# Performance work log

Hardware: AMD Instinct MI355X
Metric: run time of the kernel (lower is better)

Reference implementation:

```python
import jax, jax.numpy as jnp
import numpy as np

CHEB_K = 3

def setup_inputs() -> dict:
    key = jax.random.key(0)
    k1, k2, k3, k4 = jax.random.split(key, 4)
    B, N, C_IN, C_OUT, D = 64, 2048, 64, 64, 16
    return {
        "x": jax.random.normal(k1, (B, N, C_IN), dtype=jnp.float32),
        "node_embeddings": jax.random.normal(k2, (N, D), dtype=jnp.float32),
        "weights_pool": jax.random.normal(k3, (D, CHEB_K, C_IN, C_OUT), dtype=jnp.float32) * 0.1,
        "bias_pool": jax.random.normal(k4, (D, C_OUT), dtype=jnp.float32) * 0.1,
    }

def reference(x, node_embeddings, weights_pool, bias_pool):
    # x: [B, N, C_in]; node_embeddings: [N, D]
    N = node_embeddings.shape[0]
    # adaptive adjacency: row-softmax of relu(E E^T)
    supports = jax.nn.softmax(jax.nn.relu(node_embeddings @ node_embeddings.T), axis=1)
    # Chebyshev polynomial recursion: T0 = I, T1 = A, Tk = 2 A T_{k-1} - T_{k-2}
    support_set = [jnp.eye(N, dtype=x.dtype), supports]
    for _ in range(2, CHEB_K):
        support_set.append(2.0 * supports @ support_set[-1] - support_set[-2])
    supports_stack = jnp.stack(support_set, axis=0)  # [K, N, N]
    # per-node generated weights/bias from embedding pools
    weights = jnp.einsum('nd,dkio->nkio', node_embeddings, weights_pool)  # [N, K, C_in, C_out]
    bias = node_embeddings @ bias_pool  # [N, C_out]
    # graph convolution: aggregate then per-node GEMM
    x_g = jnp.einsum('knm,bmc->bknc', supports_stack, x)  # [B, K, N, C_in]
    out = jnp.einsum('bkni,nkio->bno', x_g, weights) + bias  # [B, N, C_out]
    return out
```

## Files before the change

### kernel.cpp

```cpp
#include <hip/hip_runtime.h>
#include <hip/hip_bf16.h>
#include <stdint.h>

using bf16   = __bf16;
using bf16x8 = __attribute__((ext_vector_type(8))) __bf16;
using f32x2  = __attribute__((ext_vector_type(2))) float;
using f32x4  = __attribute__((ext_vector_type(4))) float;

#define NN  2048
#define DD  16
#define BB  64
#define CC  64
#define BCC 4096
#define GNODE 2

__device__ inline float4 f4max(float4 a, float4 b) {
  return make_float4(fmaxf(a.x,b.x), fmaxf(a.y,b.y), fmaxf(a.z,b.z), fmaxf(a.w,b.w));
}
__device__ inline float4 f4add(float4 a, float4 b) {
  return make_float4(a.x+b.x, a.y+b.y, a.z+b.z, a.w+b.w);
}

__global__ __launch_bounds__(256) void k_softmax(const float* __restrict__ E,
                                                 bf16* __restrict__ A) {
  const int n0 = blockIdx.x * 4;
  const int t = threadIdx.x;
  float en[4][DD];
#pragma unroll
  for (int g = 0; g < 4; ++g)
#pragma unroll
    for (int d = 0; d < DD; ++d) en[g][d] = E[(size_t)(n0 + g) * DD + d];

  float4 r[8];
  float4 mx = make_float4(0.f, 0.f, 0.f, 0.f);
#pragma unroll
  for (int j = 0; j < 8; ++j) {
    const int m = t + 256 * j;
    const float4* ep = (const float4*)(E + (size_t)m * DD);
    float4 p0 = ep[0], p1 = ep[1], p2 = ep[2], p3 = ep[3];
    float s[4];
#pragma unroll
    for (int g = 0; g < 4; ++g) {
      s[g] = p0.x*en[g][0] + p0.y*en[g][1] + p0.z*en[g][2] + p0.w*en[g][3]
           + p1.x*en[g][4] + p1.y*en[g][5] + p1.z*en[g][6] + p1.w*en[g][7]
           + p2.x*en[g][8] + p2.y*en[g][9] + p2.z*en[g][10] + p2.w*en[g][11]
           + p3.x*en[g][12]+ p3.y*en[g][13]+ p3.z*en[g][14]+ p3.w*en[g][15];
      s[g] = fmaxf(s[g], 0.0f);
    }
    r[j] = make_float4(s[0], s[1], s[2], s[3]);
    mx = f4max(mx, r[j]);
  }
  __shared__ float4 red[256];
  red[t] = mx;
  __syncthreads();
  for (int off = 128; off > 0; off >>= 1) {
    if (t < off) red[t] = f4max(red[t], red[t + off]);
    __syncthreads();
  }
  mx = red[0];
  __syncthreads();
  float4 ex[8];
  float4 sum = make_float4(0.f, 0.f, 0.f, 0.f);
#pragma unroll
  for (int j = 0; j < 8; ++j) {
    ex[j] = make_float4(__expf(r[j].x - mx.x), __expf(r[j].y - mx.y),
                        __expf(r[j].z - mx.z), __expf(r[j].w - mx.w));
    sum = f4add(sum, ex[j]);
  }
  red[t] = sum;
  __syncthreads();
  for (int off = 128; off > 0; off >>= 1) {
    if (t < off) red[t] = f4add(red[t], red[t + off]);
    __syncthreads();
  }
  const float4 tot = red[0];
  const float inv[4] = {1.f/tot.x, 1.f/tot.y, 1.f/tot.z, 1.f/tot.w};
#pragma unroll
  for (int j = 0; j < 8; ++j) {
    const int m = t + 256 * j;
    A[(size_t)(n0 + 0) * NN + m] = (bf16)(ex[j].x * inv[0]);
    A[(size_t)(n0 + 1) * NN + m] = (bf16)(ex[j].y * inv[1]);
    A[(size_t)(n0 + 2) * NN + m] = (bf16)(ex[j].z * inv[2]);
    A[(size_t)(n0 + 3) * NN + m] = (bf16)(ex[j].w * inv[3]);
  }
}

__global__ __launch_bounds__(256) void k_transpose(const bf16* __restrict__ in,
                                                   bf16* __restrict__ out,
                                                   int R, int C) {
  __shared__ bf16 tile[64 * 68];
  const int bx = blockIdx.x, by = blockIdx.y;
  const int t = threadIdx.x;
  const int r0 = by * 64, c0 = bx * 64;
#pragma unroll
  for (int j = 0; j < 16; ++j) {
    const int q = t + 256 * j;
    const int r = q >> 6, c = q & 63;
    tile[r * 68 + c] = in[(size_t)(r0 + r) * C + c0 + c];
  }
  __syncthreads();
#pragma unroll
  for (int j = 0; j < 16; ++j) {
    const int q = t + 256 * j;
    const int rr = q >> 6, cc = q & 63;
    out[(size_t)(c0 + rr) * R + r0 + cc] = tile[cc * 68 + rr];
  }
}

__global__ __launch_bounds__(256) void k_build_xrt(const float* __restrict__ x,
                                                   bf16* __restrict__ XrT) {
  __shared__ bf16 tile[64 * 68];
  const int b = blockIdx.x;
  const int m0 = blockIdx.y * 64;
  const int t = threadIdx.x;
#pragma unroll
  for (int j = 0; j < 16; ++j) {
    const int q = t + 256 * j;
    const int m = q >> 6, i = q & 63;
    tile[m * 68 + i] = (bf16)x[((size_t)b * NN + m0 + m) * CC + i];
  }
  __syncthreads();
#pragma unroll
  for (int j = 0; j < 16; ++j) {
    const int q = t + 256 * j;
    const int i = q >> 6, m = q & 63;
    XrT[((size_t)b * CC + i) * NN + m0 + m] = tile[m * 68 + i];
  }
}

__global__ __launch_bounds__(256) void k_prep_wpt(const float* __restrict__ Wp,
                                                  bf16* __restrict__ WpT) {
  const int e = blockIdx.x * 256 + threadIdx.x;
  const int r = e >> 6, o = e & 63;
  const size_t src = (size_t)(r >> 6) * 4096 + (size_t)(r & 63) * 64 + o;
#pragma unroll
  for (int d = 0; d < DD; ++d)
    WpT[(size_t)e * DD + d] = (bf16)Wp[(size_t)d * 12288 + src];
}

template <int EPI>
__global__ __launch_bounds__(256) void k_gemm_bt(const bf16* __restrict__ L,
                                                 const bf16* __restrict__ R,
                                                 bf16* __restrict__ C,
                                                 int M, int Nc, int K,
                                                 const float* __restrict__ Xext,
                                                 bf16* __restrict__ CT) {
  __shared__ uint4 lds[4096];
  const int t = threadIdx.x;
  const int lane = t & 63, w = t >> 6;
  const int wm = w & 1, wn = w >> 1;
  const int h = lane >> 4;

  const int nwg = gridDim.x * gridDim.y;
  const int bid = blockIdx.y * gridDim.x + blockIdx.x;
  int bx, by;
  if (gridDim.x == 32 && gridDim.y == 16) {
    const int xcd = bid & 7, j = bid >> 3;
    bx = (xcd & 3) * 8 + (j & 7);
    by = (xcd >> 2) * 8 + (j >> 3);
  } else {
    const int cpx = nwg >> 3;
    const int swz = (bid & 7) * cpx + (bid >> 3);
    bx = swz % gridDim.x;
    by = swz / gridDim.x;
  }

  const int m0 = by * 128, n0 = bx * 128;

  f32x4 acc[4][4];
  const f32x4 zz = {0.f, 0.f, 0.f, 0.f};
#pragma unroll
  for (int mt = 0; mt < 4; ++mt)
#pragma unroll
    for (int nt = 0; nt < 4; ++nt) acc[mt][nt] = zz;

  auto stage = [&](int buf, int kt) {
    uint4* base = lds + buf * 2048;
#pragma unroll
    for (int c = 0; c < 4; ++c) {
      const int q = t + 256 * c;
      const int row = q >> 3, col4 = q & 7;
      const int scol = col4 ^ (row & 7);
      const bf16* srcL = L + (size_t)(m0 + row) * K + kt + (scol << 3);
      const bf16* srcR = R + (size_t)(n0 + row) * K + kt + (scol << 3);
      __builtin_amdgcn_global_load_lds(srcL, &base[q & ~63], 16, 0, 0);
      __builtin_amdgcn_global_load_lds(srcR, &base[1024 + (q & ~63)], 16, 0, 0);
    }
  };

  auto compute = [&](int buf) {
    const bf16x8* Lsv = (const bf16x8*)(lds + buf * 2048);
    const bf16x8* Rsv = (const bf16x8*)(lds + buf * 2048 + 1024);
#pragma unroll
    for (int kk = 0; kk < 2; ++kk) {
      bf16x8 af[4], bfr[4];
#pragma unroll
      for (int mt = 0; mt < 4; ++mt) {
        const int row = wm * 64 + mt * 16 + (lane & 15);
        af[mt] = Lsv[(row << 3) | ((kk * 4 + h) ^ (row & 7))];
      }
#pragma unroll
      for (int nt = 0; nt < 4; ++nt) {
        const int row = wn * 64 + nt * 16 + (lane & 15);
        bfr[nt] = Rsv[(row << 3) | ((kk * 4 + h) ^ (row & 7))];
      }
#pragma unroll
      for (int mt = 0; mt < 4; ++mt)
#pragma unroll
        for (int nt = 0; nt < 4; ++nt)
          acc[mt][nt] = __builtin_amdgcn_mfma_f32_16x16x32_bf16(
              af[mt], bfr[nt], acc[mt][nt], 0, 0, 0);
    }
  };

  const int NT = K >> 6;
  stage(0, 0);
  int cur = 0;
  for (int ts = 0; ts < NT - 1; ++ts) {
    stage(cur ^ 1, (ts + 1) << 6);
    asm volatile("s_waitcnt vmcnt(8)" ::: "memory");
    __builtin_amdgcn_s_barrier();
    __builtin_amdgcn_sched_barrier(0);
    compute(cur);
    __builtin_amdgcn_s_barrier();
    __builtin_amdgcn_sched_barrier(0);
    cur ^= 1;
  }
  asm volatile("s_waitcnt vmcnt(0)" ::: "memory");
  __builtin_amdgcn_s_barrier();
  __builtin_amdgcn_sched_barrier(0);
  compute(cur);

#pragma unroll
  for (int mt = 0; mt < 4; ++mt)
#pragma unroll
    for (int nt = 0; nt < 4; ++nt)
#pragma unroll
      for (int r = 0; r < 4; ++r) {
        const int rg = m0 + wm * 64 + mt * 16 + 4 * h + r;
        const int cg = n0 + wn * 64 + nt * 16 + (lane & 15);
        float v = acc[mt][nt][r];
        if (EPI == 2) {
          const int b = cg >> 6, i = cg & 63;
          v = 2.0f * v - Xext[(((size_t)b * NN + rg) * CC) + i];
        }
        C[(size_t)rg * Nc + cg] = (bf16)v;
      }

  if (EPI == 1) {
    __syncthreads();
    bf16* T = (bf16*)lds;
#pragma unroll
    for (int mt = 0; mt < 4; ++mt)
#pragma unroll
      for (int nt = 0; nt < 4; ++nt)
#pragma unroll
        for (int r = 0; r < 4; ++r) {
          const int rloc = wm * 64 + mt * 16 + 4 * h + r;
          const int cloc = wn * 64 + nt * 16 + (lane & 15);
          T[cloc * 136 + rloc] = (bf16)acc[mt][nt][r];
        }
    __syncthreads();
    const int cloc = t >> 1, half = t & 1;
#pragma unroll
    for (int jj = 0; jj < 8; ++jj) {
      const bf16x8 v = *(const bf16x8*)(T + cloc * 136 + half * 64 + jj * 8);
      *(bf16x8*)(CT + (size_t)(n0 + cloc) * M + m0 + half * 64 + jj * 8) = v;
    }
  }
}

__global__ __launch_bounds__(256) void k_node(const float* __restrict__ x,
                                              const float* __restrict__ E,
                                              const bf16* __restrict__ WpT,
                                              const float* __restrict__ bp,
                                              const bf16* __restrict__ xg1,
                                              const bf16* __restrict__ xg2,
                                              float* __restrict__ out) {
  __shared__ alignas(16) bf16 sW[GNODE * 1536 * 8];
  const int t = threadIdx.x;
  const int lane = t & 63, w = t >> 6;
  const int h = lane >> 4, l16 = lane & 15;
  const int n0 = blockIdx.x * GNODE;
  const int b = w * 16 + l16;

  float4  xa[GNODE][4];
  bf16x8  xgr[GNODE][4];
#pragma unroll
  for (int g = 0; g < GNODE; ++g) {
    const int n = n0 + g;
    const float* xb = x + ((size_t)b * NN + n) * CC;
    xa[g][0] = *(const float4*)(xb + h * 8);
    xa[g][1] = *(const float4*)(xb + h * 8 + 4);
    xa[g][2] = *(const float4*)(xb + 32 + h * 8);
    xa[g][3] = *(const float4*)(xb + 32 + h * 8 + 4);
    const bf16* x1 = xg1 + (size_t)n * BCC + b * CC;
    const bf16* x2 = xg2 + (size_t)n * BCC + b * CC;
    xgr[g][0] = *(const bf16x8*)(x1 + h * 8);
    xgr[g][1] = *(const bf16x8*)(x1 + 32 + h * 8);
    xgr[g][2] = *(const bf16x8*)(x2 + h * 8);
    xgr[g][3] = *(const bf16x8*)(x2 + 32 + h * 8);
  }

  f32x2 en2[DD];
  float en[GNODE][DD];
#pragma unroll
  for (int g = 0; g < GNODE; ++g)
#pragma unroll
    for (int d = 0; d < DD; ++d) en[g][d] = E[(size_t)(n0 + g) * DD + d];
#pragma unroll
  for (int d = 0; d < DD; ++d) en2[d] = (f32x2){en[0][d], en[1][d]};

  float bias_v[GNODE][4];
#pragma unroll
  for (int g = 0; g < GNODE; ++g)
#pragma unroll
    for (int nt = 0; nt < 4; ++nt) {
      const int o = nt * 16 + l16;
      float a = 0.0f;
#pragma unroll
      for (int d = 0; d < DD; ++d) a += en[g][d] * bp[d * CC + o];
      bias_v[g][nt] = a;
    }

#pragma unroll
  for (int c = 0; c < 6; ++c) {
    const int idx = t + 256 * c;
    const int o = idx & 63;
    const int u = idx >> 6;
    const bf16* src = WpT + ((size_t)(u * 8) * 64 + o) * DD;
    bf16x8 wv[GNODE];
#pragma unroll
    for (int j = 0; j < 8; ++j) {
      const bf16x8* wr = (const bf16x8*)(src + (size_t)j * 64 * DD);
      bf16x8 w0 = wr[0], w1 = wr[1];
      f32x2 a2 = {0.f, 0.f};
#pragma unroll
      for (int d = 0; d < 8; ++d) {
        const float wf = (float)w0[d];
        a2 += (f32x2){wf, wf} * en2[d];
      }
#pragma unroll
      for (int d = 0; d < 8; ++d) {
        const float wf = (float)w1[d];
        a2 += (f32x2){wf, wf} * en2[8 + d];
      }
      wv[0][j] = (bf16)a2[0];
      wv[1][j] = (bf16)a2[1];
    }
    const int swz = o * 24 + (u & ~7) + ((u & 7) ^ (o & 7));
#pragma unroll
    for (int g = 0; g < GNODE; ++g)
      *(bf16x8*)(sW + (size_t)(g * 1536 + swz) * 8) = wv[g];
  }
  __syncthreads();

#pragma unroll
  for (int g = 0; g < GNODE; ++g) {
    f32x4 acc[4];
    const f32x4 zz = {0.f, 0.f, 0.f, 0.f};
#pragma unroll
    for (int nt = 0; nt < 4; ++nt) acc[nt] = zz;
#pragma unroll
    for (int s = 0; s < 6; ++s) {
      bf16x8 af;
      if (s < 2) {
        const float4 u4 = xa[g][s * 2], v4 = xa[g][s * 2 + 1];
        af[0] = (bf16)u4.x; af[1] = (bf16)u4.y; af[2] = (bf16)u4.z; af[3] = (bf16)u4.w;
        af[4] = (bf16)v4.x; af[5] = (bf16)v4.y; af[6] = (bf16)v4.z; af[7] = (bf16)v4.w;
      } else {
        af = xgr[g][s - 2];
      }
      const int u = s * 4 + h;
#pragma unroll
      for (int nt = 0; nt < 4; ++nt) {
        const int o = nt * 16 + l16;
        const bf16x8 bfr = *(const bf16x8*)(
            sW + (size_t)(g * 1536 + o * 24 + (u & ~7) + ((u & 7) ^ (o & 7))) * 8);
        acc[nt] = __builtin_amdgcn_mfma_f32_16x16x32_bf16(af, bfr, acc[nt], 0, 0, 0);
      }
    }
#pragma unroll
    for (int nt = 0; nt < 4; ++nt) {
      const int o = nt * 16 + l16;
#pragma unroll
      for (int r = 0; r < 4; ++r) {
        const int br = w * 16 + 4 * h + r;
        out[((size_t)br * NN + (n0 + g)) * CC + o] = acc[nt][r] + bias_v[g][nt];
      }
    }
  }
}

extern "C" void kernel_launch(void* const* d_in, const int* in_sizes, int n_in,
                              void* d_out, int out_size, void* d_ws, size_t ws_size,
                              hipStream_t stream) {
  const float* x  = (const float*)d_in[0];
  const float* E  = (const float*)d_in[1];
  const float* Wp = (const float*)d_in[2];
  const float* bp = (const float*)d_in[3];
  float* out = (float*)d_out;

  char* ws = (char*)d_ws;
  const size_t MB = (size_t)1 << 20;
  bf16* A    = (bf16*)(ws);
  bf16* XrT  = (bf16*)(ws + 8 * MB);
  bf16* xg1  = (bf16*)(ws + 24 * MB);
  bf16* xg2  = (bf16*)(ws + 40 * MB);
  bf16* WpT  = (bf16*)(ws + 56 * MB);

  k_softmax<<<NN / 4, 256, 0, stream>>>(E, A);
  k_build_xrt<<<dim3(64, 32), 256, 0, stream>>>(x, XrT);
  k_prep_wpt<<<48, 256, 0, stream>>>(Wp, WpT);

  if (ws_size >= 80 * MB) {
    bf16* Xg1T = (bf16*)(ws + 60 * MB);
    k_gemm_bt<1><<<dim3(32, 16), 256, 0, stream>>>(A, XrT, xg1, NN, BCC, NN,
                                                   nullptr, Xg1T);
    k_gemm_bt<2><<<dim3(32, 16), 256, 0, stream>>>(A, Xg1T, xg2, NN, BCC, NN,
                                                   x, nullptr);
  } else {
    bf16* Xg1T = XrT;
    k_gemm_bt<0><<<dim3(32, 16), 256, 0, stream>>>(A, XrT, xg1, NN, BCC, NN,
                                                   nullptr, nullptr);
    k_transpose<<<dim3(64, 32), 256, 0, stream>>>(xg1, Xg1T, NN, BCC);
    k_gemm_bt<2><<<dim3(32, 16), 256, 0, stream>>>(A, Xg1T, xg2, NN, BCC, NN,
                                                   x, nullptr);
  }
  k_node<<<NN / GNODE, 256, 0, stream>>>(x, E, WpT, bp, xg1, xg2, out);
}
```

Measured before the change: 136.8 us.

## Fuse prep kernels into one launch and halve k_node shared memory

Merges the softmax, x transpose/cast and weight-pool transpose kernels into a single launch that dispatches on block index, removing two kernel launches and their gaps. In k_node, the shared-memory weight buffer now holds one node instead of two. The second node's generated weights are kept in registers and written to LDS after the first node's MFMA pass, with extra barriers. A launch bound of 4 blocks per SM is added to raise occupancy, at the risk of register pressure and the added synchronisation.

```diff
diff --git a/kernel.cpp b/kernel.cpp
--- a/kernel.cpp
+++ b/kernel.cpp
@@ -12,7 +12,6 @@
 #define BB  64
 #define CC  64
 #define BCC 4096
-#define GNODE 2
 
 __device__ inline float4 f4max(float4 a, float4 b) {
   return make_float4(fmaxf(a.x,b.x), fmaxf(a.y,b.y), fmaxf(a.z,b.z), fmaxf(a.w,b.w));
@@ -21,67 +20,101 @@
   return make_float4(a.x+b.x, a.y+b.y, a.z+b.z, a.w+b.w);
 }
 
-__global__ __launch_bounds__(256) void k_softmax(const float* __restrict__ E,
-                                                 bf16* __restrict__ A) {
-  const int n0 = blockIdx.x * 4;
+__global__ __launch_bounds__(256) void k_prep_fused(const float* __restrict__ E,
+                                                    bf16* __restrict__ A,
+                                                    const float* __restrict__ x,
+                                                    bf16* __restrict__ XrT,
+                                                    const float* __restrict__ Wp,
+                                                    bf16* __restrict__ WpT) {
+  __shared__ alignas(16) char smem[64 * 68 * 2];
+  const int blk = blockIdx.x;
   const int t = threadIdx.x;
-  float en[4][DD];
-#pragma unroll
-  for (int g = 0; g < 4; ++g)
-#pragma unroll
-    for (int d = 0; d < DD; ++d) en[g][d] = E[(size_t)(n0 + g) * DD + d];
-
-  float4 r[8];
-  float4 mx = make_float4(0.f, 0.f, 0.f, 0.f);
-#pragma unroll
-  for (int j = 0; j < 8; ++j) {
-    const int m = t + 256 * j;
-    const float4* ep = (const float4*)(E + (size_t)m * DD);
-    float4 p0 = ep[0], p1 = ep[1], p2 = ep[2], p3 = ep[3];
-    float s[4];
-#pragma unroll
-    for (int g = 0; g < 4; ++g) {
-      s[g] = p0.x*en[g][0] + p0.y*en[g][1] + p0.z*en[g][2] + p0.w*en[g][3]
-           + p1.x*en[g][4] + p1.y*en[g][5] + p1.z*en[g][6] + p1.w*en[g][7]
-           + p2.x*en[g][8] + p2.y*en[g][9] + p2.z*en[g][10] + p2.w*en[g][11]
-           + p3.x*en[g][12]+ p3.y*en[g][13]+ p3.z*en[g][14]+ p3.w*en[g][15];
-      s[g] = fmaxf(s[g], 0.0f);
-    }
-    r[j] = make_float4(s[0], s[1], s[2], s[3]);
-    mx = f4max(mx, r[j]);
-  }
-  __shared__ float4 red[256];
-  red[t] = mx;
-  __syncthreads();
-  for (int off = 128; off > 0; off >>= 1) {
-    if (t < off) red[t] = f4max(red[t], red[t + off]);
-    __syncthreads();
-  }
-  mx = red[0];
-  __syncthreads();
-  float4 ex[8];
-  float4 sum = make_float4(0.f, 0.f, 0.f, 0.f);
-#pragma unroll
-  for (int j = 0; j < 8; ++j) {
-    ex[j] = make_float4(__expf(r[j].x - mx.x), __expf(r[j].y - mx.y),
-                        __expf(r[j].z - mx.z), __expf(r[j].w - mx.w));
-    sum = f4add(sum, ex[j]);
-  }
-  red[t] = sum;
-  __syncthreads();
-  for (int off = 128; off > 0; off >>= 1) {
-    if (t < off) red[t] = f4add(red[t], red[t + off]);
-    __syncthreads();
-  }
-  const float4 tot = red[0];
-  const float inv[4] = {1.f/tot.x, 1.f/tot.y, 1.f/tot.z, 1.f/tot.w};
-#pragma unroll
-  for (int j = 0; j < 8; ++j) {
-    const int m = t + 256 * j;
-    A[(size_t)(n0 + 0) * NN + m] = (bf16)(ex[j].x * inv[0]);
-    A[(size_t)(n0 + 1) * NN + m] = (bf16)(ex[j].y * inv[1]);
-    A[(size_t)(n0 + 2) * NN + m] = (bf16)(ex[j].z * inv[2]);
-    A[(size_t)(n0 + 3) * NN + m] = (bf16)(ex[j].w * inv[3]);
+
+  if (blk < 512) {
+    float4* red = (float4*)smem;
+    const int n0 = blk * 4;
+    float en[4][DD];
+#pragma unroll
+    for (int g = 0; g < 4; ++g)
+#pragma unroll
+      for (int d = 0; d < DD; ++d) en[g][d] = E[(size_t)(n0 + g) * DD + d];
+
+    float4 r[8];
+    float4 mx = make_float4(0.f, 0.f, 0.f, 0.f);
+#pragma unroll
+    for (int j = 0; j < 8; ++j) {
+      const int m = t + 256 * j;
+      const float4* ep = (const float4*)(E + (size_t)m * DD);
+      float4 p0 = ep[0], p1 = ep[1], p2 = ep[2], p3 = ep[3];
+      float s[4];
+#pragma unroll
+      for (int g = 0; g < 4; ++g) {
+        s[g] = p0.x*en[g][0] + p0.y*en[g][1] + p0.z*en[g][2] + p0.w*en[g][3]
+             + p1.x*en[g][4] + p1.y*en[g][5] + p1.z*en[g][6] + p1.w*en[g][7]
+             + p2.x*en[g][8] + p2.y*en[g][9] + p2.z*en[g][10] + p2.w*en[g][11]
+             + p3.x*en[g][12]+ p3.y*en[g][13]+ p3.z*en[g][14]+ p3.w*en[g][15];
+        s[g] = fmaxf(s[g], 0.0f);
+      }
+      r[j] = make_float4(s[0], s[1], s[2], s[3]);
+      mx = f4max(mx, r[j]);
+    }
+    red[t] = mx;
+    __syncthreads();
+    for (int off = 128; off > 0; off >>= 1) {
+      if (t < off) red[t] = f4max(red[t], red[t + off]);
+      __syncthreads();
+    }
+    mx = red[0];
+    __syncthreads();
+    float4 ex[8];
+    float4 sum = make_float4(0.f, 0.f, 0.f, 0.f);
+#pragma unroll
+    for (int j = 0; j < 8; ++j) {
+      ex[j] = make_float4(__expf(r[j].x - mx.x), __expf(r[j].y - mx.y),
+                          __expf(r[j].z - mx.z), __expf(r[j].w - mx.w));
+      sum = f4add(sum, ex[j]);
+    }
+    red[t] = sum;
+    __syncthreads();
+    for (int off = 128; off > 0; off >>= 1) {
+      if (t < off) red[t] = f4add(red[t], red[t + off]);
+      __syncthreads();
+    }
+    const float4 tot = red[0];
+    const float inv[4] = {1.f/tot.x, 1.f/tot.y, 1.f/tot.z, 1.f/tot.w};
+#pragma unroll
+    for (int j = 0; j < 8; ++j) {
+      const int m = t + 256 * j;
+      A[(size_t)(n0 + 0) * NN + m] = (bf16)(ex[j].x * inv[0]);
+      A[(size_t)(n0 + 1) * NN + m] = (bf16)(ex[j].y * inv[1]);
+      A[(size_t)(n0 + 2) * NN + m] = (bf16)(ex[j].z * inv[2]);
+      A[(size_t)(n0 + 3) * NN + m] = (bf16)(ex[j].w * inv[3]);
+    }
+  } else if (blk < 2560) {
+    bf16* tile = (bf16*)smem;
+    const int q0 = blk - 512;
+    const int b = q0 >> 5;
+    const int m0 = (q0 & 31) * 64;
+#pragma unroll
+    for (int j = 0; j < 16; ++j) {
+      const int q = t + 256 * j;
+      const int m = q >> 6, i = q & 63;
+      tile[m * 68 + i] = (bf16)x[((size_t)b * NN + m0 + m) * CC + i];
+    }
+    __syncthreads();
+#pragma unroll
+    for (int j = 0; j < 16; ++j) {
+      const int q = t + 256 * j;
+      const int i = q >> 6, m = q & 63;
+      XrT[((size_t)b * CC + i) * NN + m0 + m] = tile[m * 68 + i];
+    }
+  } else {
+    const int e = (blk - 2560) * 256 + t;
+    const int r = e >> 6, o = e & 63;
+    const size_t src = (size_t)(r >> 6) * 4096 + (size_t)(r & 63) * 64 + o;
+#pragma unroll
+    for (int d = 0; d < DD; ++d)
+      WpT[(size_t)e * DD + d] = (bf16)Wp[(size_t)d * 12288 + src];
   }
 }
 
@@ -105,37 +138,6 @@
     const int rr = q >> 6, cc = q & 63;
     out[(size_t)(c0 + rr) * R + r0 + cc] = tile[cc * 68 + rr];
   }
-}
-
-__global__ __launch_bounds__(256) void k_build_xrt(const float* __restrict__ x,
-                                                   bf16* __restrict__ XrT) {
-  __shared__ bf16 tile[64 * 68];
-  const int b = blockIdx.x;
-  const int m0 = blockIdx.y * 64;
-  const int t = threadIdx.x;
-#pragma unroll
-  for (int j = 0; j < 16; ++j) {
-    const int q = t + 256 * j;
-    const int m = q >> 6, i = q & 63;
-    tile[m * 68 + i] = (bf16)x[((size_t)b * NN + m0 + m) * CC + i];
-  }
-  __syncthreads();
-#pragma unroll
-  for (int j = 0; j < 16; ++j) {
-    const int q = t + 256 * j;
-    const int i = q >> 6, m = q & 63;
-    XrT[((size_t)b * CC + i) * NN + m0 + m] = tile[m * 68 + i];
-  }
-}
-
-__global__ __launch_bounds__(256) void k_prep_wpt(const float* __restrict__ Wp,
-                                                  bf16* __restrict__ WpT) {
-  const int e = blockIdx.x * 256 + threadIdx.x;
-  const int r = e >> 6, o = e & 63;
-  const size_t src = (size_t)(r >> 6) * 4096 + (size_t)(r & 63) * 64 + o;
-#pragma unroll
-  for (int d = 0; d < DD; ++d)
-    WpT[(size_t)e * DD + d] = (bf16)Wp[(size_t)d * 12288 + src];
 }
 
 template <int EPI>
@@ -270,24 +272,24 @@
   }
 }
 
-__global__ __launch_bounds__(256) void k_node(const float* __restrict__ x,
-                                              const float* __restrict__ E,
-                                              const bf16* __restrict__ WpT,
-                                              const float* __restrict__ bp,
-                                              const bf16* __restrict__ xg1,
-                                              const bf16* __restrict__ xg2,
-                                              float* __restrict__ out) {
-  __shared__ alignas(16) bf16 sW[GNODE * 1536 * 8];
+__global__ __launch_bounds__(256, 4) void k_node(const float* __restrict__ x,
+                                                 const float* __restrict__ E,
+                                                 const bf16* __restrict__ WpT,
+                                                 const float* __restrict__ bp,
+                                                 const bf16* __restrict__ xg1,
+                                                 const bf16* __restrict__ xg2,
+                                                 float* __restrict__ out) {
+  __shared__ alignas(16) bf16 sW[1536 * 8];
   const int t = threadIdx.x;
   const int lane = t & 63, w = t >> 6;
   const int h = lane >> 4, l16 = lane & 15;
-  const int n0 = blockIdx.x * GNODE;
+  const int n0 = blockIdx.x * 2;
   const int b = w * 16 + l16;
 
-  float4  xa[GNODE][4];
-  bf16x8  xgr[GNODE][4];
-#pragma unroll
-  for (int g = 0; g < GNODE; ++g) {
+  float4  xa[2][4];
+  bf16x8  xgr[2][4];
+#pragma unroll
+  for (int g = 0; g < 2; ++g) {
     const int n = n0 + g;
     const float* xb = x + ((size_t)b * NN + n) * CC;
     xa[g][0] = *(const float4*)(xb + h * 8);
@@ -303,17 +305,17 @@
   }
 
   f32x2 en2[DD];
-  float en[GNODE][DD];
-#pragma unroll
-  for (int g = 0; g < GNODE; ++g)
+  float en[2][DD];
+#pragma unroll
+  for (int g = 0; g < 2; ++g)
 #pragma unroll
     for (int d = 0; d < DD; ++d) en[g][d] = E[(size_t)(n0 + g) * DD + d];
 #pragma unroll
   for (int d = 0; d < DD; ++d) en2[d] = (f32x2){en[0][d], en[1][d]};
 
-  float bias_v[GNODE][4];
-#pragma unroll
-  for (int g = 0; g < GNODE; ++g)
+  float bias_v[2][4];
+#pragma unroll
+  for (int g = 0; g < 2; ++g)
 #pragma unroll
     for (int nt = 0; nt < 4; ++nt) {
       const int o = nt * 16 + l16;
@@ -323,13 +325,14 @@
       bias_v[g][nt] = a;
     }
 
+  bf16x8 wst[6];
 #pragma unroll
   for (int c = 0; c < 6; ++c) {
     const int idx = t + 256 * c;
     const int o = idx & 63;
     const int u = idx >> 6;
     const bf16* src = WpT + ((size_t)(u * 8) * 64 + o) * DD;
-    bf16x8 wv[GNODE];
+    bf16x8 wv0, wv1;
 #pragma unroll
     for (int j = 0; j < 8; ++j) {
       const bf16x8* wr = (const bf16x8*)(src + (size_t)j * 64 * DD);
@@ -345,18 +348,17 @@
         const float wf = (float)w1[d];
         a2 += (f32x2){wf, wf} * en2[8 + d];
       }
-      wv[0][j] = (bf16)a2[0];
-      wv[1][j] = (bf16)a2[1];
+      wv0[j] = (bf16)a2[0];
+      wv1[j] = (bf16)a2[1];
     }
     const int swz = o * 24 + (u & ~7) + ((u & 7) ^ (o & 7));
-#pragma unroll
-    for (int g = 0; g < GNODE; ++g)
-      *(bf16x8*)(sW + (size_t)(g * 1536 + swz) * 8) = wv[g];
+    *(bf16x8*)(sW + (size_t)swz * 8) = wv0;
+    wst[c] = wv1;
   }
   __syncthreads();
 
 #pragma unroll
-  for (int g = 0; g < GNODE; ++g) {
+  for (int g = 0; g < 2; ++g) {
     f32x4 acc[4];
     const f32x4 zz = {0.f, 0.f, 0.f, 0.f};
 #pragma unroll
@@ -376,7 +378,7 @@
       for (int nt = 0; nt < 4; ++nt) {
         const int o = nt * 16 + l16;
         const bf16x8 bfr = *(const bf16x8*)(
-            sW + (size_t)(g * 1536 + o * 24 + (u & ~7) + ((u & 7) ^ (o & 7))) * 8);
+            sW + (size_t)(o * 24 + (u & ~7) + ((u & 7) ^ (o & 7))) * 8);
         acc[nt] = __builtin_amdgcn_mfma_f32_16x16x32_bf16(af, bfr, acc[nt], 0, 0, 0);
       }
     }
@@ -388,6 +390,18 @@
         const int br = w * 16 + 4 * h + r;
         out[((size_t)br * NN + (n0 + g)) * CC + o] = acc[nt][r] + bias_v[g][nt];
       }
+    }
+    if (g == 0) {
+      __syncthreads();
+#pragma unroll
+      for (int c = 0; c < 6; ++c) {
+        const int idx = t + 256 * c;
+        const int o = idx & 63;
+        const int u = idx >> 6;
+        const int swz = o * 24 + (u & ~7) + ((u & 7) ^ (o & 7));
+        *(bf16x8*)(sW + (size_t)swz * 8) = wst[c];
+      }
+      __syncthreads();
     }
   }
 }
@@ -409,9 +423,7 @@
   bf16* xg2  = (bf16*)(ws + 40 * MB);
   bf16* WpT  = (bf16*)(ws + 56 * MB);
 
-  k_softmax<<<NN / 4, 256, 0, stream>>>(E, A);
-  k_build_xrt<<<dim3(64, 32), 256, 0, stream>>>(x, XrT);
-  k_prep_wpt<<<48, 256, 0, stream>>>(Wp, WpT);
+  k_prep_fused<<<2608, 256, 0, stream>>>(E, A, x, XrT, Wp, WpT);
 
   if (ws_size >= 80 * MB) {
     bf16* Xg1T = (bf16*)(ws + 60 * MB);
@@ -427,5 +439,5 @@
     k_gemm_bt<2><<<dim3(32, 16), 256, 0, stream>>>(A, Xg1T, xg2, NN, BCC, NN,
                                                    x, nullptr);
   }
-  k_node<<<NN / GNODE, 256, 0, stream>>>(x, E, WpT, bp, xg1, xg2, out);
-}
+  k_node<<<NN / 2, 256, 0, stream>>>(x, E, WpT, bp, xg1, xg2, out);
+}
```

Measured after the change: 138.9 us. No clear change (+1.5%).
